# Kernel optimization log

Measured on AMD Instinct MI355X. Metric: run time of the kernel, lower is better.

The kernel has to match this reference:

```python
import jax, jax.numpy as jnp
import numpy as np

TAU = 0.07
K = 50
EPS = 1e-8


def _flat_norm(x):
    # [B, C, H, W] -> [B*H*W, C], L2-normalized along C
    B, C = x.shape[0], x.shape[1]
    x = jnp.moveaxis(x, 1, -1).reshape(-1, C)
    n = jnp.linalg.norm(x, axis=-1, keepdims=True)
    return x / jnp.maximum(n, 1e-12)


def setup_inputs() -> dict:
    key = jax.random.key(0)
    ks = jax.random.split(key, 5)
    shp = (2, 128, 64, 64)
    lshp = (2, 4, 64, 64)
    return {
        "input": jax.random.normal(ks[0], shp, dtype=jnp.float32),
        "positive": jax.random.normal(ks[1], shp, dtype=jnp.float32),
        "negative": jax.random.normal(ks[2], shp, dtype=jnp.float32),
        "input_logits": jax.random.normal(ks[3], lshp, dtype=jnp.float32),
        "negative_logits": jax.random.normal(ks[4], lshp, dtype=jnp.float32),
    }


def reference(input, positive, negative, input_logits, negative_logits):
    norm_input = _flat_norm(input)        # [N, C]
    norm_positive = _flat_norm(positive)  # [N, C]
    norm_negative = _flat_norm(negative)  # [N, C]

    # check_input: multi-class logits branch (softmax over class dim, then max)
    in_probs = jax.nn.softmax(input_logits, axis=1)
    neg_probs = jax.nn.softmax(negative_logits, axis=1)
    seg_input = jnp.argmax(in_probs, axis=1).reshape(-1)       # [N] int
    seg_negative = jnp.argmax(neg_probs, axis=1).reshape(-1)   # [N] int
    negative_prob = jnp.max(neg_probs, axis=1).reshape(-1)     # [N] float

    # positive cosine similarity (unit vectors -> dot product)
    pos_sim = jnp.sum(norm_input * norm_positive, axis=-1)     # [N]

    # mask[i, j] = (seg_input[j] != seg_negative[i]) * negative_prob[i]
    diff = (seg_input[None, :] != seg_negative[:, None]).astype(jnp.float16)
    masked = diff.astype(jnp.float32) * negative_prob[:, None]  # [N, N]

    # top-k over dim=0 (negatives) for each input column j -> indices [N, K]
    _, idx = jax.lax.top_k(masked.T, K)                         # [N, K]
    sampled = norm_negative[idx]                                # [N, K, C]

    neg_sim = jnp.einsum('nkc,nc->nk', sampled, norm_input)     # [N, K]
    nominator = jnp.exp(pos_sim / TAU)                          # [N]
    denominator = jnp.sum(jnp.exp(neg_sim / TAU), axis=1) + nominator
    loss = -jnp.mean(jnp.log(nominator / (denominator + EPS)))

    alter_sim = jnp.einsum('nkc,nc->nk', sampled, norm_positive)
    alter_den = jnp.sum(jnp.exp(alter_sim / TAU), axis=1) + nominator
    alter_loss = -jnp.mean(jnp.log(nominator / (alter_den + EPS)))

    return loss + alter_loss
```

## Files before the change

### kernel.cpp

```cpp
#include <hip/hip_runtime.h>
#include <math.h>

#define TAU_INV (1.0f / 0.07f)
#define KSEL 50
#define KPAD 64
#define NPIX 8192
#define CCH 128
#define HWSZ 4096
#define NCLS 4
#define EPSL 1e-8f
#define NBINS 1026
#define PXT 16
#define SROW 132

__global__ void __launch_bounds__(256) mega_kernel(
        const float* __restrict__ input, const float* __restrict__ positive,
        const float* __restrict__ negative,
        const float* __restrict__ ilog, const float* __restrict__ nlog,
        float* __restrict__ ni, float* __restrict__ np_, float* __restrict__ nn,
        int* __restrict__ seg_in, int* __restrict__ seg_neg,
        float* __restrict__ neg_prob) {
    __shared__ float tile[CCH][65];
    __shared__ float partial[4][64];
    __shared__ float invn[64];

    int t = threadIdx.x;
    int blk = blockIdx.x;

    if (blk < 384) {
        int tensor = blk >> 7, chunk = blk & 127;
        const float* src = (tensor == 0) ? input : (tensor == 1) ? positive : negative;
        float*       dst = (tensor == 0) ? ni    : (tensor == 1) ? np_      : nn;

        int n0 = chunk * 64;
        int b = n0 >> 12, hw0 = n0 & (HWSZ - 1);
        const float* base = src + (size_t)b * CCH * HWSZ + hw0;

        #pragma unroll
        for (int i = 0; i < 32; ++i) {
            int lin = t + i * 256;
            int c = lin >> 6, hw = lin & 63;
            tile[c][hw] = base[(size_t)c * HWSZ + hw];
        }
        __syncthreads();

        int nof = t & 63, part = t >> 6;
        float s = 0.f;
        #pragma unroll
        for (int j = 0; j < 32; ++j) {
            float v = tile[part * 32 + j][nof];
            s += v * v;
        }
        partial[part][nof] = s;
        __syncthreads();
        if (t < 64) {
            float tot = partial[0][t] + partial[1][t] + partial[2][t] + partial[3][t];
            invn[t] = 1.0f / fmaxf(sqrtf(tot), 1e-12f);
        }
        __syncthreads();

        #pragma unroll
        for (int i = 0; i < 32; ++i) {
            int lin = t + i * 256;
            int nf = lin >> 7, c = lin & 127;
            dst[(size_t)(n0 + nf) * CCH + c] = tile[c][nf] * invn[nf];
        }
    } else {
        int n = (blk - 384) * 256 + t;
        int b = n >> 12, hw = n & (HWSZ - 1);

        const float* pi = ilog + (size_t)b * NCLS * HWSZ + hw;
        float l0 = pi[0], l1 = pi[HWSZ], l2 = pi[2 * HWSZ], l3 = pi[3 * HWSZ];
        int bi = 0; float bv = l0;
        if (l1 > bv) { bv = l1; bi = 1; }
        if (l2 > bv) { bv = l2; bi = 2; }
        if (l3 > bv) { bv = l3; bi = 3; }
        seg_in[n] = bi;

        const float* pn = nlog + (size_t)b * NCLS * HWSZ + hw;
        float m0 = pn[0], m1 = pn[HWSZ], m2 = pn[2 * HWSZ], m3 = pn[3 * HWSZ];
        int ci = 0; float cv = m0;
        if (m1 > cv) { cv = m1; ci = 1; }
        if (m2 > cv) { cv = m2; ci = 2; }
        if (m3 > cv) { cv = m3; ci = 3; }
        seg_neg[n] = ci;
        float s = expf(m0 - cv) + expf(m1 - cv) + expf(m2 - cv) + expf(m3 - cv);
        neg_prob[n] = 1.0f / s;
    }
}

__global__ void __launch_bounds__(1024) topk_kernel(
        const int* __restrict__ seg_in, const int* __restrict__ seg_neg,
        const float* __restrict__ neg_prob,
        int* __restrict__ topk, int* __restrict__ perm, int* __restrict__ cnt,
        float* __restrict__ out) {
    __shared__ unsigned hist[NBINS];
    __shared__ unsigned coarse[33];
    __shared__ unsigned long long cand[2048];
    __shared__ unsigned above_cnt, cand_cnt, bucket_cnt;
    __shared__ int sB, sc0;

    int c = blockIdx.x, t = threadIdx.x;
    if (c == 0 && t == 0) out[0] = 0.0f;

    for (int i = t; i < NBINS; i += 1024) hist[i] = 0;
    if (t < 33) coarse[t] = 0;
    if (t == 0) { above_cnt = 0; cand_cnt = 0; bucket_cnt = 0; }
    __syncthreads();

    unsigned keys[8]; int bins[8];
    #pragma unroll
    for (int s = 0; s < 8; ++s) {
        int i = t + s * 1024;
        float v = (seg_neg[i] != c) ? neg_prob[i] : 0.0f;
        unsigned key = __float_as_uint(v);
        int bin = (key < 0x3E800000u) ? 0 : (int)(1u + ((key - 0x3E800000u) >> 14));
        keys[s] = key; bins[s] = bin;
        atomicAdd(&hist[bin], 1u);
        if (seg_in[i] == c) {
            unsigned p = atomicAdd(&bucket_cnt, 1u);
            perm[c * NPIX + p] = i;
        }
    }
    __syncthreads();
    if (t == 0) cnt[c] = (int)bucket_cnt;

    for (int i = t; i < NBINS; i += 1024) atomicAdd(&coarse[i >> 5], hist[i]);
    __syncthreads();

    if (t == 0) {
        unsigned cum = 0; int j = 32;
        for (; j > 0; --j) {
            unsigned h = coarse[j];
            if (cum + h >= KSEL) break;
            cum += h;
        }
        int hi = j * 32 + 31; if (hi > NBINS - 1) hi = NBINS - 1;
        int B = 0;
        for (int b = hi; b >= j * 32; --b) {
            unsigned h = hist[b];
            if (cum + h >= KSEL) { B = b; break; }
            cum += h;
        }
        sB = B; sc0 = (int)cum;
    }
    __syncthreads();
    int B = sB, c0 = sc0;

    #pragma unroll
    for (int s = 0; s < 8; ++s) {
        int i = t + s * 1024;
        if (bins[s] > B) {
            unsigned pos = atomicAdd(&above_cnt, 1u);
            topk[c * KSEL + pos] = i;
        } else if (bins[s] == B) {
            unsigned j = atomicAdd(&cand_cnt, 1u);
            if (j < 2048)
                cand[j] = ((unsigned long long)keys[s] << 32) |
                          (unsigned long long)(0xFFFFFFFFu - (unsigned)i);
        }
    }
    __syncthreads();

    int m = KSEL - c0;
    int cb = (int)cand_cnt; if (cb > 2048) cb = 2048;
    if (t < 64) {
        for (int r = 0; r < m; ++r) {
            unsigned long long best = 0;
            for (int j = t; j < cb; j += 64) {
                unsigned long long v = cand[j];
                if (v > best) best = v;
            }
            #pragma unroll
            for (int off = 32; off; off >>= 1) {
                unsigned long long o = __shfl_xor(best, off);
                if (o > best) best = o;
            }
            if (t == 0) topk[c * KSEL + c0 + r] = (int)(0xFFFFFFFFu - (unsigned)(best & 0xFFFFFFFFull));
            for (int j = t; j < cb; j += 64)
                if (cand[j] == best) cand[j] = 0;
        }
    }
}

__global__ void __launch_bounds__(256) loss_kernel(
        const float* __restrict__ ni, const float* __restrict__ npos,
        const float* __restrict__ nn, const int* __restrict__ topk,
        const int* __restrict__ perm, const int* __restrict__ cnt,
        float* __restrict__ out) {
    __shared__ float Sl[KPAD * SROW];
    __shared__ float Xl[PXT * SROW];
    __shared__ float Pl[PXT * SROW];
    __shared__ float bsum[4];

    int c = blockIdx.y;
    int count = cnt[c];
    int start = blockIdx.x * PXT;
    if (start >= count) return;
    int t = threadIdx.x;

    {
        int row = t >> 2;
        int ch0 = (t & 3) * 32;
        float* dst = &Sl[row * SROW + ch0];
        if (row < KSEL) {
            const float* src = nn + (size_t)topk[c * KSEL + row] * CCH + ch0;
            #pragma unroll
            for (int i = 0; i < 8; ++i)
                ((float4*)dst)[i] = ((const float4*)src)[i];
        } else {
            float4 z = make_float4(0.f, 0.f, 0.f, 0.f);
            #pragma unroll
            for (int i = 0; i < 8; ++i)
                ((float4*)dst)[i] = z;
        }
    }
    {
        int row = t >> 4;
        int slot = start + row;
        int px = perm[c * NPIX + ((slot < count) ? slot : start)];
        int ch0 = (t & 15) * 8;
        const float* sx = ni + (size_t)px * CCH + ch0;
        const float* sp = npos + (size_t)px * CCH + ch0;
        float* dx = &Xl[row * SROW + ch0];
        float* dp = &Pl[row * SROW + ch0];
        ((float4*)dx)[0] = ((const float4*)sx)[0];
        ((float4*)dx)[1] = ((const float4*)sx)[1];
        ((float4*)dp)[0] = ((const float4*)sp)[0];
        ((float4*)dp)[1] = ((const float4*)sp)[1];
    }
    __syncthreads();

    int ktid = t & 15, pxid = t >> 4;
    float acc_i[4] = {0.f, 0.f, 0.f, 0.f};
    float acc_p[4] = {0.f, 0.f, 0.f, 0.f};
    float ps = 0.f;
    const float* Xr = &Xl[pxid * SROW];
    const float* Pr = &Pl[pxid * SROW];

    #pragma unroll 4
    for (int ch = 0; ch < CCH; ch += 4) {
        float4 xv = *(const float4*)&Xr[ch];
        float4 pv = *(const float4*)&Pr[ch];
        ps += xv.x * pv.x + xv.y * pv.y + xv.z * pv.z + xv.w * pv.w;
        #pragma unroll
        for (int r = 0; r < 4; ++r) {
            float4 sv = *(const float4*)&Sl[(ktid + r * 16) * SROW + ch];
            acc_i[r] += sv.x * xv.x + sv.y * xv.y + sv.z * xv.z + sv.w * xv.w;
            acc_p[r] += sv.x * pv.x + sv.y * pv.y + sv.z * pv.z + sv.w * pv.w;
        }
    }

    float si = 0.f, spp = 0.f;
    #pragma unroll
    for (int r = 0; r < 4; ++r) {
        si  += expf(acc_i[r] * TAU_INV);
        spp += expf(acc_p[r] * TAU_INV);
    }
    #pragma unroll
    for (int off = 1; off < 16; off <<= 1) {
        si  += __shfl_xor(si, off);
        spp += __shfl_xor(spp, off);
    }

    float v = 0.f;
    if (ktid == 0 && (start + pxid) < count) {
        si  -= (float)(KPAD - KSEL);
        spp -= (float)(KPAD - KSEL);
        float nom = expf(ps * TAU_INV);
        float li = -logf(nom / (si + nom + EPSL));
        float lp = -logf(nom / (spp + nom + EPSL));
        v = (li + lp) * (1.0f / (float)NPIX);
    }
    v += __shfl_xor(v, 16);
    v += __shfl_xor(v, 32);
    int w = t >> 6;
    if ((t & 63) == 0) bsum[w] = v;
    __syncthreads();
    if (t == 0) atomicAdd(out, bsum[0] + bsum[1] + bsum[2] + bsum[3]);
}

extern "C" void kernel_launch(void* const* d_in, const int* in_sizes, int n_in,
                              void* d_out, int out_size, void* d_ws, size_t ws_size,
                              hipStream_t stream) {
    const float* input      = (const float*)d_in[0];
    const float* positive   = (const float*)d_in[1];
    const float* negative   = (const float*)d_in[2];
    const float* in_logits  = (const float*)d_in[3];
    const float* neg_logits = (const float*)d_in[4];
    float* out = (float*)d_out;

    float* ws  = (float*)d_ws;
    float* ni  = ws;
    float* np_ = ws + 1048576;
    float* nn  = ws + 2097152;
    int*   seg_in   = (int*)(ws + 3145728);
    int*   seg_neg  = seg_in + NPIX;
    float* neg_prob = (float*)(seg_neg + NPIX);
    int*   topk     = (int*)(neg_prob + NPIX);
    int*   cnt      = topk + 256;
    int*   perm     = cnt + 64;

    mega_kernel<<<416, 256, 0, stream>>>(input, positive, negative,
                                         in_logits, neg_logits,
                                         ni, np_, nn, seg_in, seg_neg, neg_prob);
    topk_kernel<<<NCLS, 1024, 0, stream>>>(seg_in, seg_neg, neg_prob,
                                           topk, perm, cnt, out);
    dim3 lgrid(NPIX / PXT, NCLS);
    loss_kernel<<<lgrid, 256, 0, stream>>>(ni, np_, nn, topk, perm, cnt, out);
}
```

Baseline: 101.8 us.

## Vectorize loads/stores with float4 and double pixels per loss block

Switches the normalization, logits argmax and top-k input reads to float4/int4 vector accesses. Each thread now handles four logits pixels, which cuts the logits-block count from 32 to 8. The loss kernel goes from 16 to 32 pixels per block, with each thread accumulating 8 negatives instead of 4, so each staged negative tile is reused more. In exchange, registers per thread rise and there are half as many loss blocks. The top-k scan order changes, so candidate ordering and the reconstruction of pixel indices have to stay consistent.

```diff
diff --git a/kernel.cpp b/kernel.cpp
--- a/kernel.cpp
+++ b/kernel.cpp
@@ -10,7 +10,7 @@
 #define NCLS 4
 #define EPSL 1e-8f
 #define NBINS 1026
-#define PXT 16
+#define PXT 32
 #define SROW 132
 
 __global__ void __launch_bounds__(256) mega_kernel(
@@ -37,10 +37,12 @@
         const float* base = src + (size_t)b * CCH * HWSZ + hw0;
 
         #pragma unroll
-        for (int i = 0; i < 32; ++i) {
+        for (int i = 0; i < 8; ++i) {
             int lin = t + i * 256;
-            int c = lin >> 6, hw = lin & 63;
-            tile[c][hw] = base[(size_t)c * HWSZ + hw];
+            int c = lin >> 4, hwq = (lin & 15) * 4;
+            float4 v = *(const float4*)&base[(size_t)c * HWSZ + hwq];
+            tile[c][hwq + 0] = v.x; tile[c][hwq + 1] = v.y;
+            tile[c][hwq + 2] = v.z; tile[c][hwq + 3] = v.w;
         }
         __syncthreads();
 
@@ -60,32 +62,58 @@
         __syncthreads();
 
         #pragma unroll
-        for (int i = 0; i < 32; ++i) {
+        for (int i = 0; i < 8; ++i) {
             int lin = t + i * 256;
-            int nf = lin >> 7, c = lin & 127;
-            dst[(size_t)(n0 + nf) * CCH + c] = tile[c][nf] * invn[nf];
+            int nf = lin >> 5, cq = (lin & 31) * 4;
+            float inv = invn[nf];
+            float4 o;
+            o.x = tile[cq + 0][nf] * inv;
+            o.y = tile[cq + 1][nf] * inv;
+            o.z = tile[cq + 2][nf] * inv;
+            o.w = tile[cq + 3][nf] * inv;
+            *(float4*)&dst[(size_t)(n0 + nf) * CCH + cq] = o;
         }
     } else {
-        int n = (blk - 384) * 256 + t;
-        int b = n >> 12, hw = n & (HWSZ - 1);
+        int n0 = ((blk - 384) * 256 + t) * 4;
+        int b = n0 >> 12, hw = n0 & (HWSZ - 1);
 
         const float* pi = ilog + (size_t)b * NCLS * HWSZ + hw;
-        float l0 = pi[0], l1 = pi[HWSZ], l2 = pi[2 * HWSZ], l3 = pi[3 * HWSZ];
-        int bi = 0; float bv = l0;
-        if (l1 > bv) { bv = l1; bi = 1; }
-        if (l2 > bv) { bv = l2; bi = 2; }
-        if (l3 > bv) { bv = l3; bi = 3; }
-        seg_in[n] = bi;
-
+        float4 a0 = *(const float4*)&pi[0];
+        float4 a1 = *(const float4*)&pi[HWSZ];
+        float4 a2 = *(const float4*)&pi[2 * HWSZ];
+        float4 a3 = *(const float4*)&pi[3 * HWSZ];
         const float* pn = nlog + (size_t)b * NCLS * HWSZ + hw;
-        float m0 = pn[0], m1 = pn[HWSZ], m2 = pn[2 * HWSZ], m3 = pn[3 * HWSZ];
-        int ci = 0; float cv = m0;
-        if (m1 > cv) { cv = m1; ci = 1; }
-        if (m2 > cv) { cv = m2; ci = 2; }
-        if (m3 > cv) { cv = m3; ci = 3; }
-        seg_neg[n] = ci;
-        float s = expf(m0 - cv) + expf(m1 - cv) + expf(m2 - cv) + expf(m3 - cv);
-        neg_prob[n] = 1.0f / s;
+        float4 b0 = *(const float4*)&pn[0];
+        float4 b1 = *(const float4*)&pn[HWSZ];
+        float4 b2 = *(const float4*)&pn[2 * HWSZ];
+        float4 b3 = *(const float4*)&pn[3 * HWSZ];
+
+        int4 si4, sn4; float4 npb;
+        const float* A0 = (const float*)&a0; const float* A1 = (const float*)&a1;
+        const float* A2 = (const float*)&a2; const float* A3 = (const float*)&a3;
+        const float* B0 = (const float*)&b0; const float* B1 = (const float*)&b1;
+        const float* B2 = (const float*)&b2; const float* B3 = (const float*)&b3;
+        int* SI = (int*)&si4; int* SN = (int*)&sn4; float* NP = (float*)&npb;
+        #pragma unroll
+        for (int j = 0; j < 4; ++j) {
+            float l0 = A0[j], l1 = A1[j], l2 = A2[j], l3 = A3[j];
+            int bi = 0; float bv = l0;
+            if (l1 > bv) { bv = l1; bi = 1; }
+            if (l2 > bv) { bv = l2; bi = 2; }
+            if (l3 > bv) { bv = l3; bi = 3; }
+            SI[j] = bi;
+            float m0 = B0[j], m1 = B1[j], m2 = B2[j], m3 = B3[j];
+            int ci = 0; float cv = m0;
+            if (m1 > cv) { cv = m1; ci = 1; }
+            if (m2 > cv) { cv = m2; ci = 2; }
+            if (m3 > cv) { cv = m3; ci = 3; }
+            SN[j] = ci;
+            float s = expf(m0 - cv) + expf(m1 - cv) + expf(m2 - cv) + expf(m3 - cv);
+            NP[j] = 1.0f / s;
+        }
+        *(int4*)&seg_in[n0] = si4;
+        *(int4*)&seg_neg[n0] = sn4;
+        *(float4*)&neg_prob[n0] = npb;
     }
 }
 
@@ -110,16 +138,25 @@
 
     unsigned keys[8]; int bins[8];
     #pragma unroll
-    for (int s = 0; s < 8; ++s) {
-        int i = t + s * 1024;
-        float v = (seg_neg[i] != c) ? neg_prob[i] : 0.0f;
-        unsigned key = __float_as_uint(v);
-        int bin = (key < 0x3E800000u) ? 0 : (int)(1u + ((key - 0x3E800000u) >> 14));
-        keys[s] = key; bins[s] = bin;
-        atomicAdd(&hist[bin], 1u);
-        if (seg_in[i] == c) {
-            unsigned p = atomicAdd(&bucket_cnt, 1u);
-            perm[c * NPIX + p] = i;
+    for (int s = 0; s < 2; ++s) {
+        int i4 = (t + s * 1024) * 4;
+        int4 sn = *(const int4*)&seg_neg[i4];
+        int4 sg = *(const int4*)&seg_in[i4];
+        float4 npv = *(const float4*)&neg_prob[i4];
+        const int* SN = (const int*)&sn;
+        const int* SG = (const int*)&sg;
+        const float* NP = (const float*)&npv;
+        #pragma unroll
+        for (int j = 0; j < 4; ++j) {
+            float v = (SN[j] != c) ? NP[j] : 0.0f;
+            unsigned key = __float_as_uint(v);
+            int bin = (key < 0x3E800000u) ? 0 : (int)(1u + ((key - 0x3E800000u) >> 14));
+            keys[s * 4 + j] = key; bins[s * 4 + j] = bin;
+            atomicAdd(&hist[bin], 1u);
+            if (SG[j] == c) {
+                unsigned p = atomicAdd(&bucket_cnt, 1u);
+                perm[c * NPIX + p] = i4 + j;
+            }
         }
     }
     __syncthreads();
@@ -149,7 +186,7 @@
 
     #pragma unroll
     for (int s = 0; s < 8; ++s) {
-        int i = t + s * 1024;
+        int i = (t + (s >> 2) * 1024) * 4 + (s & 3);
         if (bins[s] > B) {
             unsigned pos = atomicAdd(&above_cnt, 1u);
             topk[c * KSEL + pos] = i;
@@ -216,36 +253,37 @@
         }
     }
     {
-        int row = t >> 4;
+        int row = t >> 3;
         int slot = start + row;
         int px = perm[c * NPIX + ((slot < count) ? slot : start)];
-        int ch0 = (t & 15) * 8;
+        int ch0 = (t & 7) * 16;
         const float* sx = ni + (size_t)px * CCH + ch0;
         const float* sp = npos + (size_t)px * CCH + ch0;
         float* dx = &Xl[row * SROW + ch0];
         float* dp = &Pl[row * SROW + ch0];
-        ((float4*)dx)[0] = ((const float4*)sx)[0];
-        ((float4*)dx)[1] = ((const float4*)sx)[1];
-        ((float4*)dp)[0] = ((const float4*)sp)[0];
-        ((float4*)dp)[1] = ((const float4*)sp)[1];
-    }
-    __syncthreads();
-
-    int ktid = t & 15, pxid = t >> 4;
-    float acc_i[4] = {0.f, 0.f, 0.f, 0.f};
-    float acc_p[4] = {0.f, 0.f, 0.f, 0.f};
+        #pragma unroll
+        for (int i = 0; i < 4; ++i) {
+            ((float4*)dx)[i] = ((const float4*)sx)[i];
+            ((float4*)dp)[i] = ((const float4*)sp)[i];
+        }
+    }
+    __syncthreads();
+
+    int ktid = t & 7, pxid = t >> 3;
+    float acc_i[8] = {0.f, 0.f, 0.f, 0.f, 0.f, 0.f, 0.f, 0.f};
+    float acc_p[8] = {0.f, 0.f, 0.f, 0.f, 0.f, 0.f, 0.f, 0.f};
     float ps = 0.f;
     const float* Xr = &Xl[pxid * SROW];
     const float* Pr = &Pl[pxid * SROW];
 
-    #pragma unroll 4
+    #pragma unroll 2
     for (int ch = 0; ch < CCH; ch += 4) {
         float4 xv = *(const float4*)&Xr[ch];
         float4 pv = *(const float4*)&Pr[ch];
         ps += xv.x * pv.x + xv.y * pv.y + xv.z * pv.z + xv.w * pv.w;
         #pragma unroll
-        for (int r = 0; r < 4; ++r) {
-            float4 sv = *(const float4*)&Sl[(ktid + r * 16) * SROW + ch];
+        for (int r = 0; r < 8; ++r) {
+            float4 sv = *(const float4*)&Sl[(ktid + r * 8) * SROW + ch];
             acc_i[r] += sv.x * xv.x + sv.y * xv.y + sv.z * xv.z + sv.w * xv.w;
             acc_p[r] += sv.x * pv.x + sv.y * pv.y + sv.z * pv.z + sv.w * pv.w;
         }
@@ -253,12 +291,12 @@
 
     float si = 0.f, spp = 0.f;
     #pragma unroll
-    for (int r = 0; r < 4; ++r) {
+    for (int r = 0; r < 8; ++r) {
         si  += expf(acc_i[r] * TAU_INV);
         spp += expf(acc_p[r] * TAU_INV);
     }
     #pragma unroll
-    for (int off = 1; off < 16; off <<= 1) {
+    for (int off = 1; off < 8; off <<= 1) {
         si  += __shfl_xor(si, off);
         spp += __shfl_xor(spp, off);
     }
@@ -272,6 +310,7 @@
         float lp = -logf(nom / (spp + nom + EPSL));
         v = (li + lp) * (1.0f / (float)NPIX);
     }
+    v += __shfl_xor(v, 8);
     v += __shfl_xor(v, 16);
     v += __shfl_xor(v, 32);
     int w = t >> 6;
@@ -301,7 +340,7 @@
     int*   cnt      = topk + 256;
     int*   perm     = cnt + 64;
 
-    mega_kernel<<<416, 256, 0, stream>>>(input, positive, negative,
+    mega_kernel<<<392, 256, 0, stream>>>(input, positive, negative,
                                          in_logits, neg_logits,
                                          ni, np_, nn, seg_in, seg_neg, neg_prob);
     topk_kernel<<<NCLS, 1024, 0, stream>>>(seg_in, seg_neg, neg_prob,
```

Result: faster. 99.72 us (median of 2 runs) (-2.1%).
